# Optimization experiments

Hardware: AMD Instinct MI355X
Metric: run time of the kernel (lower is better)

The kernel has to match this reference:

```python
import jax, jax.numpy as jnp
import numpy as np

N_NODES = 100000
N_EDGES = 1600000
IN_C = 64
HID = 32
OUT_C = 32
NEG_SLOPE = 0.2  # PyG GATConv default


def _gat_layer(x, src, dst, W, a_src, a_dst, b, n_nodes):
    # h: [N, F]; src/dst include self-loops
    h = x @ W
    # edge logits: att_src on source node, att_dst on target node (PyG convention)
    e = jax.nn.leaky_relu((h @ a_src)[src] + (h @ a_dst)[dst], NEG_SLOPE)
    # segment softmax grouped by target node
    m = jax.ops.segment_max(e, dst, num_segments=n_nodes)
    ex = jnp.exp(e - m[dst])
    denom = jax.ops.segment_sum(ex, dst, num_segments=n_nodes)
    alpha = ex / denom[dst]
    # scatter-aggregate weighted messages at target nodes
    out = jax.ops.segment_sum(alpha[:, None] * h[src], dst, num_segments=n_nodes)
    return out + b


def setup_inputs() -> dict:
    key = jax.random.key(0)
    ks = jax.random.split(key, 16)
    x = jax.random.normal(ks[0], (N_NODES, IN_C), dtype=jnp.float32)
    edge_index = jax.random.randint(ks[1], (2, N_EDGES), 0, N_NODES, dtype=jnp.int32)

    def glorot(k, shape):
        lim = float(np.sqrt(6.0 / (shape[0] + shape[-1])))
        return jax.random.uniform(k, shape, jnp.float32, -lim, lim)

    d1 = 2 * HID  # 64
    return {
        "x": x,
        "edge_index": edge_index,
        "W1": glorot(ks[2], (IN_C, d1)),
        "att_src1": glorot(ks[3], (d1,)),
        "att_dst1": glorot(ks[4], (d1,)),
        "b1": jnp.zeros((d1,), jnp.float32),
        "W2": glorot(ks[5], (d1, HID)),
        "att_src2": glorot(ks[6], (HID,)),
        "att_dst2": glorot(ks[7], (HID,)),
        "b2": jnp.zeros((HID,), jnp.float32),
        "W3": glorot(ks[8], (HID, OUT_C)),
        "att_src3": glorot(ks[9], (OUT_C,)),
        "att_dst3": glorot(ks[10], (OUT_C,)),
        "b3": jnp.zeros((OUT_C,), jnp.float32),
        "threshold_distance": jnp.asarray(10.0, jnp.float32),
        "cansu": jnp.asarray(0.75, jnp.float32),
    }


def reference(x, edge_index, W1, att_src1, att_dst1, b1, W2, att_src2, att_dst2, b2,
              W3, att_src3, att_dst3, b3, threshold_distance, cansu):
    n = x.shape[0]
    loops = jnp.arange(n, dtype=edge_index.dtype)
    src = jnp.concatenate([edge_index[0], loops])  # add self-loops (PyG default)
    dst = jnp.concatenate([edge_index[1], loops])
    td = threshold_distance * cansu
    h = jax.nn.relu(_gat_layer(x, src, dst, W1, att_src1, att_dst1, b1, n))
    h = jax.nn.relu(_gat_layer(h, src, dst, W2, att_src2, att_dst2, b2, n))
    h = _gat_layer(h, src, dst, W3, att_src3, att_dst3, b3, n) * td
    return jnp.mean(h, axis=0, keepdims=True)  # batch=None path -> [1, out]
```

## Files before the change

kernel.cpp:

```cpp
#include <hip/hip_runtime.h>


constexpr int BLOCK = 256;
constexpr int NBLK = 512;
constexpr int BSH = 6;
constexpr int MAXNB = 1600;

__device__ __forceinline__ float llrelu(float x) { return x >= 0.f ? x : 0.2f * x; }

__device__ __forceinline__ unsigned short f2bf(float f) {
    unsigned int u = __float_as_uint(f);
    u += 0x7FFFu + ((u >> 16) & 1u);
    return (unsigned short)(u >> 16);
}
__device__ __forceinline__ float bf2f(unsigned short h) {
    return __uint_as_float((unsigned int)h << 16);
}

template <int FIN, int FOUT, bool RELU_IN>
__device__ __forceinline__ void gemm_att_body(
    const float* __restrict__ X, const float* __restrict__ W,
    const float* __restrict__ asrc, const float* __restrict__ adst,
    unsigned short* __restrict__ H, float* __restrict__ Ssrc,
    float* __restrict__ Sdst, int n, int gblk, float* Xs, float* Ws) {
    constexpr int CG = FOUT / 4;
    constexpr int NG = BLOCK / CG;
    constexpr int TN = NG * 4;
    constexpr int S = FIN + 4;

    int tid = threadIdx.x;
    int n0_blk = gblk * TN;

    for (int t = tid; t < FIN * FOUT / 4; t += BLOCK) {
        float4 v = ((const float4*)W)[t];
        *(float4*)&Ws[t * 4] = v;
    }
    constexpr int RW = FIN / 4;
    for (int t = tid; t < TN * RW; t += BLOCK) {
        int r = t / RW, c = t % RW;
        int gr = n0_blk + r;
        if (gr >= n) gr = n - 1;
        float4 v = ((const float4*)(X + (size_t)gr * FIN))[c];
        if (RELU_IN) {
            v.x = fmaxf(v.x, 0.f); v.y = fmaxf(v.y, 0.f);
            v.z = fmaxf(v.z, 0.f); v.w = fmaxf(v.w, 0.f);
        }
        *(float4*)&Xs[r * S + c * 4] = v;
    }
    __syncthreads();

    int tx = tid % CG, ty = tid / CG;
    int c0 = tx * 4, nloc = ty * 4;

    float acc[4][4];
#pragma unroll
    for (int i = 0; i < 4; ++i)
#pragma unroll
        for (int j = 0; j < 4; ++j) acc[i][j] = 0.f;

#pragma unroll 2
    for (int kc = 0; kc < FIN / 4; ++kc) {
        float4 xv[4], wv[4];
#pragma unroll
        for (int i = 0; i < 4; ++i) xv[i] = *(const float4*)&Xs[(nloc + i) * S + kc * 4];
#pragma unroll
        for (int kk = 0; kk < 4; ++kk) wv[kk] = *(const float4*)&Ws[(kc * 4 + kk) * FOUT + c0];
#pragma unroll
        for (int i = 0; i < 4; ++i) {
            float xi0 = xv[i].x, xi1 = xv[i].y, xi2 = xv[i].z, xi3 = xv[i].w;
            acc[i][0] = fmaf(xi0, wv[0].x, acc[i][0]);
            acc[i][1] = fmaf(xi0, wv[0].y, acc[i][1]);
            acc[i][2] = fmaf(xi0, wv[0].z, acc[i][2]);
            acc[i][3] = fmaf(xi0, wv[0].w, acc[i][3]);
            acc[i][0] = fmaf(xi1, wv[1].x, acc[i][0]);
            acc[i][1] = fmaf(xi1, wv[1].y, acc[i][1]);
            acc[i][2] = fmaf(xi1, wv[1].z, acc[i][2]);
            acc[i][3] = fmaf(xi1, wv[1].w, acc[i][3]);
            acc[i][0] = fmaf(xi2, wv[2].x, acc[i][0]);
            acc[i][1] = fmaf(xi2, wv[2].y, acc[i][1]);
            acc[i][2] = fmaf(xi2, wv[2].z, acc[i][2]);
            acc[i][3] = fmaf(xi2, wv[2].w, acc[i][3]);
            acc[i][0] = fmaf(xi3, wv[3].x, acc[i][0]);
            acc[i][1] = fmaf(xi3, wv[3].y, acc[i][1]);
            acc[i][2] = fmaf(xi3, wv[3].z, acc[i][2]);
            acc[i][3] = fmaf(xi3, wv[3].w, acc[i][3]);
        }
    }

    float4 as4 = *(const float4*)&asrc[c0];
    float4 ad4 = *(const float4*)&adst[c0];

#pragma unroll
    for (int i = 0; i < 4; ++i) {
        int node = n0_blk + nloc + i;
        bool ok = node < n;
        if (ok) {
            ushort4 hb;
            hb.x = f2bf(acc[i][0]); hb.y = f2bf(acc[i][1]);
            hb.z = f2bf(acc[i][2]); hb.w = f2bf(acc[i][3]);
            *(ushort4*)&H[(size_t)node * FOUT + c0] = hb;
        }
        float vs = acc[i][0] * as4.x + acc[i][1] * as4.y + acc[i][2] * as4.z + acc[i][3] * as4.w;
        float vd = acc[i][0] * ad4.x + acc[i][1] * ad4.y + acc[i][2] * ad4.z + acc[i][3] * ad4.w;
#pragma unroll
        for (int off = CG / 2; off > 0; off >>= 1) {
            vs += __shfl_xor(vs, off, CG);
            vd += __shfl_xor(vd, off, CG);
        }
        if (tx == 0 && ok) {
            Ssrc[node] = vs;
            Sdst[node] = vd;
        }
    }
}

template <int FIN, int FOUT, bool RELU_IN>
__global__ void gemm_att_kernel(const float* __restrict__ X, const float* __restrict__ W,
                                const float* __restrict__ asrc, const float* __restrict__ adst,
                                unsigned short* __restrict__ H, float* __restrict__ Ssrc,
                                float* __restrict__ Sdst, int n) {
    constexpr int CG = FOUT / 4;
    constexpr int NG = BLOCK / CG;
    constexpr int TN = NG * 4;
    constexpr int S = FIN + 4;
    __shared__ float Xs[TN * S];
    __shared__ float Ws[FIN * FOUT];
    gemm_att_body<FIN, FOUT, RELU_IN>(X, W, asrc, adst, H, Ssrc, Sdst, n, blockIdx.x, Xs, Ws);
}

__global__ void hist_gemm1_kernel(const float* __restrict__ X, const float* __restrict__ W,
                                  const float* __restrict__ asrc, const float* __restrict__ adst,
                                  unsigned short* __restrict__ H, float* __restrict__ Ssrc,
                                  float* __restrict__ Sdst, int n, int ngemm,
                                  const int* __restrict__ dst, int E, int chunk, int NB,
                                  int* __restrict__ S, float* __restrict__ facc) {
    __shared__ __align__(16) float lds[8448];
    int bid = blockIdx.x;
    if ((bid & 1) == 0) {
        int gb = bid >> 1;
        if (gb >= ngemm) return;
        gemm_att_body<64, 64, false>(X, W, asrc, adst, H, Ssrc, Sdst, n, gb, lds, lds + 64 * 68);
    } else {
        int k = bid >> 1;
        if (k >= NBLK) return;
        int* hist = (int*)lds;
        for (int i = threadIdx.x; i < NB; i += BLOCK) hist[i] = 0;
        if (k == 0 && threadIdx.x < 32) facc[threadIdx.x] = 0.f;
        __syncthreads();
        int start = k * chunk, end = min(E, start + chunk);
        for (int i = start + threadIdx.x; i < end; i += BLOCK)
            atomicAdd(&hist[dst[i] >> BSH], 1);
        __syncthreads();
        for (int b = threadIdx.x; b < NB; b += BLOCK) S[(size_t)b * NBLK + k] = hist[b];
    }
}

__global__ void scan1_kernel(int* __restrict__ S, int total, int* __restrict__ bsums) {
    __shared__ int s[1024];
    int tid = threadIdx.x;
    int gid = blockIdx.x * 1024 + tid;
    int v = (gid < total) ? S[gid] : 0;
    s[tid] = v;
    for (int off = 1; off < 1024; off <<= 1) {
        __syncthreads();
        int t = (tid >= off) ? s[tid - off] : 0;
        __syncthreads();
        s[tid] += t;
    }
    __syncthreads();
    if (gid < total) S[gid] = s[tid] - v;
    if (tid == 1023) bsums[blockIdx.x] = s[tid];
}

__global__ void scan2_kernel(int* __restrict__ bsums, int nb) {
    __shared__ int s[1024];
    __shared__ int carry_s;
    int tid = threadIdx.x;
    if (tid == 0) carry_s = 0;
    __syncthreads();
    for (int base = 0; base < nb; base += 1024) {
        int i = base + tid;
        int v = (i < nb) ? bsums[i] : 0;
        s[tid] = v;
        for (int off = 1; off < 1024; off <<= 1) {
            __syncthreads();
            int t = (tid >= off) ? s[tid - off] : 0;
            __syncthreads();
            s[tid] += t;
        }
        __syncthreads();
        int c = carry_s;
        if (i < nb) bsums[i] = s[tid] - v + c;
        __syncthreads();
        if (tid == 1023) carry_s = c + s[1023];
        __syncthreads();
    }
}

__global__ void scan3_kernel(int* __restrict__ S, const int* __restrict__ bsums, int total) {
    int gid = blockIdx.x * blockDim.x + threadIdx.x;
    if (gid < total) S[gid] += bsums[gid >> 10];
}

__global__ void scatter_kernel(const int* __restrict__ src, const int* __restrict__ dst,
                               int E, int chunk, int NB, const int* __restrict__ S,
                               int* __restrict__ pairs) {
    __shared__ int cursor[MAXNB];
    int k = blockIdx.x;
    for (int b = threadIdx.x; b < NB; b += BLOCK) cursor[b] = S[(size_t)b * NBLK + k];
    __syncthreads();
    int start = k * chunk, end = min(E, start + chunk);
    for (int i = start + threadIdx.x; i < end; i += BLOCK) {
        int d = dst[i], s = src[i];
        int pos = atomicAdd(&cursor[d >> BSH], 1);
        pairs[pos] = s | ((d & 63) << 17);
    }
}

__global__ void bucket_csr_kernel(const int* __restrict__ pairs, const int* __restrict__ S,
                                  int NB, int n, int E, int* __restrict__ rowst,
                                  int* __restrict__ esrc) {
    __shared__ int cnt[64], excl[64];
    int b = blockIdx.x;
    if (b >= NB) return;
    int base = S[(size_t)b * NBLK];
    int end = (b + 1 < NB) ? S[(size_t)(b + 1) * NBLK] : E;
    int m = end - base;
    if (threadIdx.x < 64) cnt[threadIdx.x] = 0;
    __syncthreads();
    for (int i = threadIdx.x; i < m; i += BLOCK)
        atomicAdd(&cnt[pairs[base + i] >> 17], 1);
    __syncthreads();
    if (threadIdx.x == 0) {
        int run = 0;
        for (int j = 0; j < 64; ++j) { excl[j] = run; run += cnt[j]; }
    }
    __syncthreads();
    int node0 = b << BSH;
    if (threadIdx.x < 64) {
        int node = node0 + threadIdx.x;
        if (node < n) rowst[node] = base + excl[threadIdx.x];
        cnt[threadIdx.x] = excl[threadIdx.x];
    }
    if (b == NB - 1 && threadIdx.x == 0) rowst[n] = E;
    __syncthreads();
    for (int i = threadIdx.x; i < m; i += BLOCK) {
        int p = pairs[base + i];
        int pos = atomicAdd(&cnt[p >> 17], 1);
        esrc[base + pos] = p & 0x1FFFF;
    }
}

template <int NBATCH>
__device__ __forceinline__ void gather_fma2(const unsigned int* __restrict__ Hu,
                                            const float* wldsg, const int* ildsg,
                                            int j0, int lane, float& acc0, float& acc1) {
    float wv[NBATCH];
    int ix[NBATCH];
#pragma unroll
    for (int q = 0; q < NBATCH / 4; ++q) {
        float4 w = *(const float4*)&wldsg[j0 + q * 4];
        int4 i4 = *(const int4*)&ildsg[j0 + q * 4];
        wv[q * 4 + 0] = w.x; wv[q * 4 + 1] = w.y; wv[q * 4 + 2] = w.z; wv[q * 4 + 3] = w.w;
        ix[q * 4 + 0] = i4.x; ix[q * 4 + 1] = i4.y; ix[q * 4 + 2] = i4.z; ix[q * 4 + 3] = i4.w;
    }
    unsigned int pv[NBATCH];
#pragma unroll
    for (int u = 0; u < NBATCH; ++u) pv[u] = Hu[(size_t)(unsigned)(ix[u] + lane)];
#pragma unroll
    for (int u = 0; u < NBATCH; ++u) {
        acc0 = fmaf(wv[u], __uint_as_float(pv[u] << 16), acc0);
        acc1 = fmaf(wv[u], __uint_as_float(pv[u] & 0xFFFF0000u), acc1);
    }
}

template <int F, int K>
__device__ __forceinline__ float2 aggr_node_core(
    const unsigned short* __restrict__ H, const float* __restrict__ Ssrc,
    const float* __restrict__ Sdst, const int* __restrict__ row_start,
    const int* __restrict__ esrc, int node, int lane,
    float* wldsg, int* ildsg) {
    constexpr int LPN = F / 2;
    constexpr int NS = K * LPN;
    const unsigned int* Hu = (const unsigned int*)H;
    int rs = row_start[node];
    int deg = row_start[node + 1] - rs;
    float sdi = Sdst[node];
    float selft = llrelu(Ssrc[node] + sdi);

    float wreg[K];
#pragma unroll
    for (int k = 0; k < K; ++k) {
        wldsg[k * LPN + lane] = 0.f;
        ildsg[k * LPN + lane] = node * LPN;
    }

    float m = selft;
#pragma unroll
    for (int k = 0; k < K; ++k) {
        int j = k * LPN + lane;
        if (j < deg) {
            int s = esrc[rs + j];
            float t = llrelu(Ssrc[s] + sdi);
            ildsg[j] = s * LPN;
            wreg[k] = t;
            m = fmaxf(m, t);
        }
    }
    for (int j = NS + lane; j < deg; j += LPN)
        m = fmaxf(m, llrelu(Ssrc[esrc[rs + j]] + sdi));
#pragma unroll
    for (int off = LPN / 2; off > 0; off >>= 1) m = fmaxf(m, __shfl_xor(m, off, LPN));

    float selfw = __expf(selft - m);
    float l = (lane == 0) ? selfw : 0.f;
#pragma unroll
    for (int k = 0; k < K; ++k) {
        int j = k * LPN + lane;
        if (j < deg) {
            float e = __expf(wreg[k] - m);
            wldsg[j] = e;
            l += e;
        }
    }
    for (int j = NS + lane; j < deg; j += LPN)
        l += __expf(llrelu(Ssrc[esrc[rs + j]] + sdi) - m);
#pragma unroll
    for (int off = LPN / 2; off > 0; off >>= 1) l += __shfl_xor(l, off, LPN);
    float winv = 1.f / l;

    unsigned int pself = Hu[(size_t)node * LPN + lane];
    float acc0 = selfw * __uint_as_float(pself << 16);
    float acc1 = selfw * __uint_as_float(pself & 0xFFFF0000u);
    int nbv = deg < NS ? deg : NS;
    int nb16 = nbv & ~15;
    int j0 = 0;
    for (; j0 < nb16; j0 += 16) gather_fma2<16>(Hu, wldsg, ildsg, j0, lane, acc0, acc1);
    int rem = nbv - nb16;
    if (rem > 8) gather_fma2<16>(Hu, wldsg, ildsg, j0, lane, acc0, acc1);
    else if (rem > 0) gather_fma2<8>(Hu, wldsg, ildsg, j0, lane, acc0, acc1);

    for (int j = NS; j < deg; ++j) {
        int s = esrc[rs + j];
        float wj = __expf(llrelu(Ssrc[s] + sdi) - m);
        unsigned int p = Hu[(size_t)s * LPN + lane];
        acc0 = fmaf(wj, __uint_as_float(p << 16), acc0);
        acc1 = fmaf(wj, __uint_as_float(p & 0xFFFF0000u), acc1);
    }
    return make_float2(acc0 * winv, acc1 * winv);
}

template <int F, int K, bool WITH_BIAS>
__global__ void gat_aggr_kernel(const unsigned short* __restrict__ H,
                                const float* __restrict__ Ssrc, const float* __restrict__ Sdst,
                                const int* __restrict__ rowst, const int* __restrict__ esrc,
                                const float* __restrict__ bias, float* __restrict__ OUT, int n) {
    constexpr int LPN = F / 2;
    constexpr int GPB = BLOCK / LPN;
    __shared__ __align__(16) float wlds[GPB][K * LPN];
    __shared__ __align__(16) int ilds[GPB][K * LPN];
    int tid = threadIdx.x;
    int grp = tid / LPN, lane = tid % LPN;
    int node = blockIdx.x * GPB + grp;
    if (node >= n) return;
    float2 acc = aggr_node_core<F, K>(H, Ssrc, Sdst, rowst, esrc, node, lane,
                                      wlds[grp], ilds[grp]);
    if (WITH_BIAS) {
        float2 bb = *(const float2*)&bias[2 * lane];
        acc.x += bb.x;
        acc.y += bb.y;
    }
    *(float2*)&OUT[(size_t)node * F + 2 * lane] = acc;
}

__global__ void mean_kernel(const float* __restrict__ B, float* __restrict__ facc, int n) {
    __shared__ float s[32];
    int lane = threadIdx.x & 31, row = threadIdx.x >> 5;
    float a = 0.f;
    for (int node = blockIdx.x * 8 + row; node < n; node += gridDim.x * 8)
        a += B[(size_t)node * 32 + lane];
    if (threadIdx.x < 32) s[threadIdx.x] = 0.f;
    __syncthreads();
    atomicAdd(&s[lane], a);
    __syncthreads();
    if (threadIdx.x < 32) atomicAdd(&facc[threadIdx.x], s[threadIdx.x]);
}

__global__ void finalize_kernel(const float* __restrict__ facc, const float* __restrict__ b,
                                const float* __restrict__ tdp, const float* __restrict__ cansup,
                                float* __restrict__ out, int n) {
    int f = threadIdx.x;
    if (f < 32) {
        float td = tdp[0] * cansup[0];
        out[f] = (facc[f] / (float)n + b[f]) * td;
    }
}

extern "C" void kernel_launch(void* const* d_in, const int* in_sizes, int n_in,
                              void* d_out, int out_size, void* d_ws, size_t ws_size,
                              hipStream_t stream) {
    const float* x      = (const float*)d_in[0];
    const int* eidx     = (const int*)d_in[1];
    const float* W1     = (const float*)d_in[2];
    const float* as1    = (const float*)d_in[3];
    const float* ad1    = (const float*)d_in[4];
    const float* b1     = (const float*)d_in[5];
    const float* W2     = (const float*)d_in[6];
    const float* as2    = (const float*)d_in[7];
    const float* ad2    = (const float*)d_in[8];
    const float* b2     = (const float*)d_in[9];
    const float* W3     = (const float*)d_in[10];
    const float* as3    = (const float*)d_in[11];
    const float* ad3    = (const float*)d_in[12];
    const float* b3     = (const float*)d_in[13];
    const float* tdp    = (const float*)d_in[14];
    const float* cansup = (const float*)d_in[15];

    const int n = in_sizes[0] / 64;
    const int E = in_sizes[1] / 2;
    const int* srcp = eidx;
    const int* dstp = eidx + E;

    const int NB = (n + 63) >> BSH;
    const int chunk = (E + NBLK - 1) / NBLK;
    const int total = NB * NBLK;

    char* ws = (char*)d_ws;
    size_t off = 0;
    auto alloc = [&](size_t bytes) -> void* {
        void* p = ws + off;
        off += (bytes + 255) & ~(size_t)255;
        return p;
    };
    unsigned short* H1 = (unsigned short*)alloc((size_t)n * 64 * sizeof(unsigned short));
    unsigned short* H2 = (unsigned short*)alloc((size_t)n * 32 * sizeof(unsigned short));
    unsigned short* H3 = (unsigned short*)alloc((size_t)n * 32 * sizeof(unsigned short));
    float* B      = (float*)alloc((size_t)n * 64 * sizeof(float));
    float* ssA    = (float*)alloc((size_t)n * sizeof(float));
    float* sdA    = (float*)alloc((size_t)n * sizeof(float));
    float* ssB    = (float*)alloc((size_t)n * sizeof(float));
    float* sdB    = (float*)alloc((size_t)n * sizeof(float));
    float* ssC    = (float*)alloc((size_t)n * sizeof(float));
    float* sdC    = (float*)alloc((size_t)n * sizeof(float));
    int*   S      = (int*)alloc((size_t)total * sizeof(int));
    int*   bsums  = (int*)alloc(1024 * sizeof(int));
    int*   rowst  = (int*)alloc((size_t)(n + 1) * sizeof(int));
    int*   esrc   = (int*)alloc((size_t)E * sizeof(int));
    int*   pairs  = (int*)alloc((size_t)E * sizeof(int));
    float* facc   = (float*)alloc(64 * sizeof(float));

    const int ngemm1 = (n + 63) / 64;
    const int gmax = (ngemm1 > NBLK) ? ngemm1 : NBLK;
    hist_gemm1_kernel<<<2 * gmax, BLOCK, 0, stream>>>(
        x, W1, as1, ad1, H1, ssA, sdA, n, ngemm1, dstp, E, chunk, NB, S, facc);
    int nb1 = (total + 1023) / 1024;
    scan1_kernel<<<nb1, 1024, 0, stream>>>(S, total, bsums);
    scan2_kernel<<<1, 1024, 0, stream>>>(bsums, nb1);
    scan3_kernel<<<(total + 255) / 256, 256, 0, stream>>>(S, bsums, total);
    scatter_kernel<<<NBLK, BLOCK, 0, stream>>>(srcp, dstp, E, chunk, NB, S, pairs);
    bucket_csr_kernel<<<NB, BLOCK, 0, stream>>>(pairs, S, NB, n, E, rowst, esrc);

    gat_aggr_kernel<64, 4, true><<<(n + 7) / 8, BLOCK, 0, stream>>>(
        H1, ssA, sdA, rowst, esrc, b1, B, n);

    gemm_att_kernel<64, 32, true><<<(n + 127) / 128, BLOCK, 0, stream>>>(
        B, W2, as2, ad2, H2, ssB, sdB, n);
    gat_aggr_kernel<32, 8, true><<<(n + 15) / 16, BLOCK, 0, stream>>>(
        H2, ssB, sdB, rowst, esrc, b2, B, n);

    gemm_att_kernel<32, 32, true><<<(n + 127) / 128, BLOCK, 0, stream>>>(
        B, W3, as3, ad3, H3, ssC, sdC, n);
    gat_aggr_kernel<32, 8, false><<<(n + 15) / 16, BLOCK, 0, stream>>>(
        H3, ssC, sdC, rowst, esrc, nullptr, B, n);
    mean_kernel<<<1024, 256, 0, stream>>>(B, facc, n);
    finalize_kernel<<<1, 64, 0, stream>>>(facc, b3, tdp, cansup, (float*)d_out, n);
}
```

Measured before the change: 215.1 us.

## Fuse scan fixup into consumers, widen layer-1 gather, fuse final aggregation with mean

Removes the scan3 pass by adding block carry sums where the scatter and bucket kernels read offsets. Layer-1 aggregation now has each lane gather 4 bf16 channels (uint2), so 16 lanes cover a node and each block handles 16 nodes. The last aggregation is fused with the mean reduction: node outputs are summed in shared memory and atomically added to facc, so the output buffer is never written and reread. The intent is fewer launches and less global traffic, at the cost of more shared-memory atomics in the final layer.

```diff
diff --git a/kernel.cpp b/kernel.cpp
--- a/kernel.cpp
+++ b/kernel.cpp
@@ -12,9 +12,6 @@
     unsigned int u = __float_as_uint(f);
     u += 0x7FFFu + ((u >> 16) & 1u);
     return (unsigned short)(u >> 16);
-}
-__device__ __forceinline__ float bf2f(unsigned short h) {
-    return __uint_as_float((unsigned int)h << 16);
 }
 
 template <int FIN, int FOUT, bool RELU_IN>
@@ -197,17 +194,15 @@
     }
 }
 
-__global__ void scan3_kernel(int* __restrict__ S, const int* __restrict__ bsums, int total) {
-    int gid = blockIdx.x * blockDim.x + threadIdx.x;
-    if (gid < total) S[gid] += bsums[gid >> 10];
-}
-
 __global__ void scatter_kernel(const int* __restrict__ src, const int* __restrict__ dst,
                                int E, int chunk, int NB, const int* __restrict__ S,
-                               int* __restrict__ pairs) {
+                               const int* __restrict__ bsums, int* __restrict__ pairs) {
     __shared__ int cursor[MAXNB];
     int k = blockIdx.x;
-    for (int b = threadIdx.x; b < NB; b += BLOCK) cursor[b] = S[(size_t)b * NBLK + k];
+    for (int b = threadIdx.x; b < NB; b += BLOCK) {
+        int cell = b * NBLK + k;
+        cursor[b] = S[cell] + bsums[cell >> 10];
+    }
     __syncthreads();
     int start = k * chunk, end = min(E, start + chunk);
     for (int i = start + threadIdx.x; i < end; i += BLOCK) {
@@ -218,13 +213,18 @@
 }
 
 __global__ void bucket_csr_kernel(const int* __restrict__ pairs, const int* __restrict__ S,
-                                  int NB, int n, int E, int* __restrict__ rowst,
-                                  int* __restrict__ esrc) {
+                                  const int* __restrict__ bsums, int NB, int n, int E,
+                                  int* __restrict__ rowst, int* __restrict__ esrc) {
     __shared__ int cnt[64], excl[64];
     int b = blockIdx.x;
     if (b >= NB) return;
-    int base = S[(size_t)b * NBLK];
-    int end = (b + 1 < NB) ? S[(size_t)(b + 1) * NBLK] : E;
+    int g0 = b * NBLK;
+    int base = S[g0] + bsums[g0 >> 10];
+    int end = E;
+    if (b + 1 < NB) {
+        int g1 = (b + 1) * NBLK;
+        end = S[g1] + bsums[g1 >> 10];
+    }
     int m = end - base;
     if (threadIdx.x < 64) cnt[threadIdx.x] = 0;
     __syncthreads();
@@ -251,10 +251,25 @@
     }
 }
 
-template <int NBATCH>
-__device__ __forceinline__ void gather_fma2(const unsigned int* __restrict__ Hu,
-                                            const float* wldsg, const int* ildsg,
-                                            int j0, int lane, float& acc0, float& acc1) {
+template <int CPL> struct GatherT;
+template <> struct GatherT<2> { using T = unsigned int; };
+template <> struct GatherT<4> { using T = uint2; };
+
+__device__ __forceinline__ void unpack_fma(unsigned int p, float w, float* acc) {
+    acc[0] = fmaf(w, __uint_as_float(p << 16), acc[0]);
+    acc[1] = fmaf(w, __uint_as_float(p & 0xFFFF0000u), acc[1]);
+}
+__device__ __forceinline__ void unpack_fma(uint2 p, float w, float* acc) {
+    acc[0] = fmaf(w, __uint_as_float(p.x << 16), acc[0]);
+    acc[1] = fmaf(w, __uint_as_float(p.x & 0xFFFF0000u), acc[1]);
+    acc[2] = fmaf(w, __uint_as_float(p.y << 16), acc[2]);
+    acc[3] = fmaf(w, __uint_as_float(p.y & 0xFFFF0000u), acc[3]);
+}
+
+template <int NBATCH, typename GT>
+__device__ __forceinline__ void gather_fma_b(const GT* __restrict__ Hg,
+                                             const float* wldsg, const int* ildsg,
+                                             int j0, int lane, float* acc) {
     float wv[NBATCH];
     int ix[NBATCH];
 #pragma unroll
@@ -264,25 +279,23 @@
         wv[q * 4 + 0] = w.x; wv[q * 4 + 1] = w.y; wv[q * 4 + 2] = w.z; wv[q * 4 + 3] = w.w;
         ix[q * 4 + 0] = i4.x; ix[q * 4 + 1] = i4.y; ix[q * 4 + 2] = i4.z; ix[q * 4 + 3] = i4.w;
     }
-    unsigned int pv[NBATCH];
-#pragma unroll
-    for (int u = 0; u < NBATCH; ++u) pv[u] = Hu[(size_t)(unsigned)(ix[u] + lane)];
-#pragma unroll
-    for (int u = 0; u < NBATCH; ++u) {
-        acc0 = fmaf(wv[u], __uint_as_float(pv[u] << 16), acc0);
-        acc1 = fmaf(wv[u], __uint_as_float(pv[u] & 0xFFFF0000u), acc1);
-    }
-}
-
-template <int F, int K>
-__device__ __forceinline__ float2 aggr_node_core(
+    GT pv[NBATCH];
+#pragma unroll
+    for (int u = 0; u < NBATCH; ++u) pv[u] = Hg[(size_t)(unsigned)(ix[u] + lane)];
+#pragma unroll
+    for (int u = 0; u < NBATCH; ++u) unpack_fma(pv[u], wv[u], acc);
+}
+
+template <int F, int K, int CPL>
+__device__ __forceinline__ void aggr_node_core(
     const unsigned short* __restrict__ H, const float* __restrict__ Ssrc,
     const float* __restrict__ Sdst, const int* __restrict__ row_start,
     const int* __restrict__ esrc, int node, int lane,
-    float* wldsg, int* ildsg) {
-    constexpr int LPN = F / 2;
+    float* wldsg, int* ildsg, float* accOut) {
+    constexpr int LPN = F / CPL;
     constexpr int NS = K * LPN;
-    const unsigned int* Hu = (const unsigned int*)H;
+    using GT = typename GatherT<CPL>::T;
+    const GT* Hg = (const GT*)H;
     int rs = row_start[node];
     int deg = row_start[node + 1] - rs;
     float sdi = Sdst[node];
@@ -329,33 +342,36 @@
     for (int off = LPN / 2; off > 0; off >>= 1) l += __shfl_xor(l, off, LPN);
     float winv = 1.f / l;
 
-    unsigned int pself = Hu[(size_t)node * LPN + lane];
-    float acc0 = selfw * __uint_as_float(pself << 16);
-    float acc1 = selfw * __uint_as_float(pself & 0xFFFF0000u);
+    float acc[CPL];
+#pragma unroll
+    for (int c = 0; c < CPL; ++c) acc[c] = 0.f;
+    GT pself = Hg[(size_t)node * LPN + lane];
+    unpack_fma(pself, selfw, acc);
+
     int nbv = deg < NS ? deg : NS;
     int nb16 = nbv & ~15;
     int j0 = 0;
-    for (; j0 < nb16; j0 += 16) gather_fma2<16>(Hu, wldsg, ildsg, j0, lane, acc0, acc1);
+    for (; j0 < nb16; j0 += 16) gather_fma_b<16, GT>(Hg, wldsg, ildsg, j0, lane, acc);
     int rem = nbv - nb16;
-    if (rem > 8) gather_fma2<16>(Hu, wldsg, ildsg, j0, lane, acc0, acc1);
-    else if (rem > 0) gather_fma2<8>(Hu, wldsg, ildsg, j0, lane, acc0, acc1);
+    if (rem > 8) gather_fma_b<16, GT>(Hg, wldsg, ildsg, j0, lane, acc);
+    else if (rem > 0) gather_fma_b<8, GT>(Hg, wldsg, ildsg, j0, lane, acc);
 
     for (int j = NS; j < deg; ++j) {
         int s = esrc[rs + j];
         float wj = __expf(llrelu(Ssrc[s] + sdi) - m);
-        unsigned int p = Hu[(size_t)s * LPN + lane];
-        acc0 = fmaf(wj, __uint_as_float(p << 16), acc0);
-        acc1 = fmaf(wj, __uint_as_float(p & 0xFFFF0000u), acc1);
-    }
-    return make_float2(acc0 * winv, acc1 * winv);
-}
-
-template <int F, int K, bool WITH_BIAS>
+        GT p = Hg[(size_t)s * LPN + lane];
+        unpack_fma(p, wj, acc);
+    }
+#pragma unroll
+    for (int c = 0; c < CPL; ++c) accOut[c] = acc[c] * winv;
+}
+
+template <int F, int K, int CPL, bool WITH_BIAS>
 __global__ void gat_aggr_kernel(const unsigned short* __restrict__ H,
                                 const float* __restrict__ Ssrc, const float* __restrict__ Sdst,
                                 const int* __restrict__ rowst, const int* __restrict__ esrc,
                                 const float* __restrict__ bias, float* __restrict__ OUT, int n) {
-    constexpr int LPN = F / 2;
+    constexpr int LPN = F / CPL;
     constexpr int GPB = BLOCK / LPN;
     __shared__ __align__(16) float wlds[GPB][K * LPN];
     __shared__ __align__(16) int ilds[GPB][K * LPN];
@@ -363,27 +379,48 @@
     int grp = tid / LPN, lane = tid % LPN;
     int node = blockIdx.x * GPB + grp;
     if (node >= n) return;
-    float2 acc = aggr_node_core<F, K>(H, Ssrc, Sdst, rowst, esrc, node, lane,
-                                      wlds[grp], ilds[grp]);
+    float acc[CPL];
+    aggr_node_core<F, K, CPL>(H, Ssrc, Sdst, rowst, esrc, node, lane,
+                              wlds[grp], ilds[grp], acc);
     if (WITH_BIAS) {
-        float2 bb = *(const float2*)&bias[2 * lane];
-        acc.x += bb.x;
-        acc.y += bb.y;
-    }
-    *(float2*)&OUT[(size_t)node * F + 2 * lane] = acc;
-}
-
-__global__ void mean_kernel(const float* __restrict__ B, float* __restrict__ facc, int n) {
-    __shared__ float s[32];
-    int lane = threadIdx.x & 31, row = threadIdx.x >> 5;
-    float a = 0.f;
-    for (int node = blockIdx.x * 8 + row; node < n; node += gridDim.x * 8)
-        a += B[(size_t)node * 32 + lane];
-    if (threadIdx.x < 32) s[threadIdx.x] = 0.f;
-    __syncthreads();
-    atomicAdd(&s[lane], a);
-    __syncthreads();
-    if (threadIdx.x < 32) atomicAdd(&facc[threadIdx.x], s[threadIdx.x]);
+#pragma unroll
+        for (int c = 0; c < CPL; ++c) acc[c] += bias[CPL * lane + c];
+    }
+    if constexpr (CPL == 4) {
+        float4 v = make_float4(acc[0], acc[1], acc[2], acc[3]);
+        *(float4*)&OUT[(size_t)node * F + 4 * lane] = v;
+    } else {
+        float2 v = make_float2(acc[0], acc[1]);
+        *(float2*)&OUT[(size_t)node * F + 2 * lane] = v;
+    }
+}
+
+__global__ void aggr3_mean_kernel(const unsigned short* __restrict__ H3,
+                                  const float* __restrict__ ssC, const float* __restrict__ sdC,
+                                  const int* __restrict__ rowst, const int* __restrict__ esrc,
+                                  float* __restrict__ facc, int n) {
+    constexpr int F = 32, K = 8, CPL = 2;
+    constexpr int LPN = F / CPL;
+    constexpr int GPB = BLOCK / LPN;
+    __shared__ __align__(16) float wlds[GPB][K * LPN];
+    __shared__ __align__(16) int ilds[GPB][K * LPN];
+    __shared__ float smean[32];
+    int tid = threadIdx.x;
+    int grp = tid / LPN, lane = tid % LPN;
+    int node = blockIdx.x * GPB + grp;
+
+    if (tid < 32) smean[tid] = 0.f;
+    __syncthreads();
+
+    if (node < n) {
+        float acc[CPL];
+        aggr_node_core<F, K, CPL>(H3, ssC, sdC, rowst, esrc, node, lane,
+                                  wlds[grp], ilds[grp], acc);
+        atomicAdd(&smean[2 * lane], acc[0]);
+        atomicAdd(&smean[2 * lane + 1], acc[1]);
+    }
+    __syncthreads();
+    if (tid < 32) atomicAdd(&facc[tid], smean[tid]);
 }
 
 __global__ void finalize_kernel(const float* __restrict__ facc, const float* __restrict__ b,
@@ -456,22 +493,20 @@
     int nb1 = (total + 1023) / 1024;
     scan1_kernel<<<nb1, 1024, 0, stream>>>(S, total, bsums);
     scan2_kernel<<<1, 1024, 0, stream>>>(bsums, nb1);
-    scan3_kernel<<<(total + 255) / 256, 256, 0, stream>>>(S, bsums, total);
-    scatter_kernel<<<NBLK, BLOCK, 0, stream>>>(srcp, dstp, E, chunk, NB, S, pairs);
-    bucket_csr_kernel<<<NB, BLOCK, 0, stream>>>(pairs, S, NB, n, E, rowst, esrc);
-
-    gat_aggr_kernel<64, 4, true><<<(n + 7) / 8, BLOCK, 0, stream>>>(
+    scatter_kernel<<<NBLK, BLOCK, 0, stream>>>(srcp, dstp, E, chunk, NB, S, bsums, pairs);
+    bucket_csr_kernel<<<NB, BLOCK, 0, stream>>>(pairs, S, bsums, NB, n, E, rowst, esrc);
+
+    gat_aggr_kernel<64, 8, 4, true><<<(n + 15) / 16, BLOCK, 0, stream>>>(
         H1, ssA, sdA, rowst, esrc, b1, B, n);
 
     gemm_att_kernel<64, 32, true><<<(n + 127) / 128, BLOCK, 0, stream>>>(
         B, W2, as2, ad2, H2, ssB, sdB, n);
-    gat_aggr_kernel<32, 8, true><<<(n + 15) / 16, BLOCK, 0, stream>>>(
+    gat_aggr_kernel<32, 8, 2, true><<<(n + 15) / 16, BLOCK, 0, stream>>>(
         H2, ssB, sdB, rowst, esrc, b2, B, n);
 
     gemm_att_kernel<32, 32, true><<<(n + 127) / 128, BLOCK, 0, stream>>>(
         B, W3, as3, ad3, H3, ssC, sdC, n);
-    gat_aggr_kernel<32, 8, false><<<(n + 15) / 16, BLOCK, 0, stream>>>(
-        H3, ssC, sdC, rowst, esrc, nullptr, B, n);
-    mean_kernel<<<1024, 256, 0, stream>>>(B, facc, n);
+    aggr3_mean_kernel<<<(n + 15) / 16, BLOCK, 0, stream>>>(
+        H3, ssC, sdC, rowst, esrc, facc, n);
     finalize_kernel<<<1, 64, 0, stream>>>(facc, b3, tdp, cansup, (float*)d_out, n);
 }
```

Measured after the change: 263.1 us. 1.22x slower.
